# Kernel tuning notes

Measured on AMD Instinct MI355X. Metric: run time of the kernel, lower is better.

Reference implementation:

```python
import jax, jax.numpy as jnp
import numpy as np

NUM_CLASSES = 22
SKIP = 20            # skip_pixels: stride over flattened pixel index
N_STEPS = 200        # discretized steps along each voting ray
STEP = 4.0           # pixels per ray step
INLIER_T = 0.9       # inlier_threshold on direction dot-product
LABEL_T = 500.0      # label_threshold: min #pixels of a class to be valid


def _hough_forward(label_2d, vertex_pred, extents, poses, meta_data):
    B, H, W = label_2d.shape
    C = NUM_CLASSES
    HW = H * W

    # ---- strided pixel sampling (skip_pixels) ----
    idx = jnp.arange(0, HW, SKIP)                      # [P]
    P = idx.shape[0]
    ys = (idx // W).astype(jnp.float32)                # [P]
    xs = (idx % W).astype(jnp.float32)
    labels = label_2d.reshape(B, HW)[:, idx].astype(jnp.int32)   # [B,P]
    vp = vertex_pred.reshape(B, HW, C, 3)[:, idx]                # [B,P,C,3]
    # pick each pixel's predicted (dx,dy,z) for its own class label
    sel = jnp.take_along_axis(
        vp, jnp.broadcast_to(labels[:, :, None, None], (B, P, 1, 3)), axis=2
    )[:, :, 0]                                                   # [B,P,3]
    d = sel[..., :2]
    dn = d / (jnp.linalg.norm(d, axis=-1, keepdims=True) + 1e-9)  # unit dir [B,P,2]
    z = sel[..., 2]                                               # [B,P]
    fg = labels > 0                                               # foreground mask

    # ---- ray voting into per-class Hough accumulator ----
    t = (jnp.arange(N_STEPS, dtype=jnp.float32) + 1.0) * STEP     # [T]
    cx = xs[None, :, None] + dn[..., 0:1] * t[None, None, :]      # [B,P,T]
    cy = ys[None, :, None] + dn[..., 1:2] * t[None, None, :]
    cxi = jnp.round(cx).astype(jnp.int32)
    cyi = jnp.round(cy).astype(jnp.int32)
    inb = (cxi >= 0) & (cxi < W) & (cyi >= 0) & (cyi < H) & fg[..., None]
    cxi = jnp.clip(cxi, 0, W - 1)
    cyi = jnp.clip(cyi, 0, H - 1)
    bidx = jnp.arange(B, dtype=jnp.int32)[:, None, None]
    flat = ((bidx * C + labels[:, :, None]) * H + cyi) * W + cxi  # [B,P,T]
    hough = jnp.zeros((B * C * HW,), jnp.float32)
    hough = hough.at[flat.reshape(-1)].add(inb.reshape(-1).astype(jnp.float32))
    hough = hough.reshape(B, C, H, W)

    # ---- per-class peak ----
    hflat = hough.reshape(B, C, HW)
    vmax = hflat.max(-1)                               # [B,C]
    pk = jnp.argmax(hflat, axis=-1).astype(jnp.int32)  # [B,C]
    pky = (pk // W).astype(jnp.float32)
    pkx = (pk % W).astype(jnp.float32)

    # ---- validity: enough labeled pixels for the class ----
    b2 = jnp.arange(B, dtype=jnp.int32)[:, None]
    counts = jnp.zeros((B, C), jnp.float32).at[
        jnp.broadcast_to(b2, (B, HW)).reshape(-1),
        label_2d.reshape(-1).astype(jnp.int32),
    ].add(1.0)                                          # [B,C] full-res pixel counts
    cls_ids = jnp.arange(C, dtype=jnp.float32)
    valid = (counts >= LABEL_T) & (cls_ids[None, :] > 0)  # [B,C]

    # ---- inlier selection + inlier-averaged depth ----
    cx_c = jnp.take_along_axis(pkx, labels, axis=1)    # [B,P] peak of pixel's class
    cy_c = jnp.take_along_axis(pky, labels, axis=1)
    dvec = jnp.stack([cx_c - xs[None, :], cy_c - ys[None, :]], axis=-1)
    dvec = dvec / (jnp.linalg.norm(dvec, axis=-1, keepdims=True) + 1e-9)
    dot = jnp.sum(dn * dvec, axis=-1)                  # [B,P]
    inl = (fg & (dot > INLIER_T)).astype(jnp.float32)  # [B,P]
    bP = jnp.broadcast_to(b2, (B, P)).reshape(-1)
    z_sum = jnp.zeros((B, C), jnp.float32).at[bP, labels.reshape(-1)].add((z * inl).reshape(-1))
    n_inl = jnp.zeros((B, C), jnp.float32).at[bP, labels.reshape(-1)].add(inl.reshape(-1))
    depth = z_sum / jnp.maximum(n_inl, 1.0)            # [B,C]
    z_safe = jnp.where(jnp.abs(depth) > 1e-3, depth, 1.0)

    # ---- bbox from extents + intrinsics ----
    fx = meta_data[:, 0:1]                             # [B,1]
    fy = meta_data[:, 4:5]
    diam = jnp.linalg.norm(extents, axis=-1)[None, :]  # [1,C]
    half_w = 0.5 * diam * fx / z_safe
    half_h = 0.5 * diam * fy / z_safe
    vmask = valid.astype(jnp.float32)
    rois = jnp.stack([
        jnp.broadcast_to(b2.astype(jnp.float32), (B, C)),
        jnp.broadcast_to(cls_ids[None, :], (B, C)),
        pkx - half_w, pky - half_h, pkx + half_w, pky + half_h,
        vmax,
    ], axis=-1) * vmask[..., None]                     # [B,C,7]

    # ---- pose init: identity quaternion + backprojected translation ----
    Kinv = meta_data[:, 9:18].reshape(B, 3, 3)
    hom = jnp.stack([pkx, pky, jnp.ones_like(pkx)], axis=-1)      # [B,C,3]
    ray = jnp.einsum('bij,bcj->bci', Kinv, hom)
    T = depth[..., None] * ray                                    # [B,C,3]
    quat = jnp.broadcast_to(jnp.array([1.0, 0.0, 0.0, 0.0], jnp.float32), (B, C, 4))
    pose_out = jnp.concatenate([quat, T], axis=-1) * vmask[..., None]  # [B,C,7]

    return jnp.concatenate([rois, pose_out], axis=-1)  # [B,C,14]


def setup_inputs() -> dict:
    key = jax.random.key(0)
    k1, k2, k3 = jax.random.split(key, 3)
    B, H, W = 2, 480, 640
    label_2d = jax.random.randint(k1, (B, H, W), 0, NUM_CLASSES, dtype=jnp.int32)
    vertex_pred = jax.random.normal(k2, (B, H, W, 3 * NUM_CLASSES), dtype=jnp.float32)
    extents = jax.random.uniform(k3, (NUM_CLASSES, 3), minval=0.05, maxval=0.3, dtype=jnp.float32)
    poses = jnp.zeros((B, 13), jnp.float32)
    K = np.array([[1066.778, 0, 312.9869], [0, 1067.487, 241.3109], [0, 0, 1]], dtype=np.float32)
    Kinv = np.linalg.pinv(K).astype(np.float32)
    md = np.zeros((B, 48), np.float32)
    md[:, 0:9] = K.flatten()
    md[:, 9:18] = Kinv.flatten()
    meta_data = jnp.asarray(md)
    return {"label_2d": label_2d, "vertex_pred": vertex_pred, "extents": extents,
            "poses": poses, "meta_data": meta_data}


def reference(label_2d, vertex_pred, extents, poses, meta_data):
    return _hough_forward(label_2d, vertex_pred, extents, poses, meta_data)
```

## Files before the change

kernel.cpp:

```cpp
#include <hip/hip_runtime.h>
#include <math.h>

#define C_      22
#define SKIP_   20
#define NSTEP_  200
#define STEP_   4.0f
#define INL_T_  0.9f
#define LAB_T_  500
#define B_      2
#define H_      480
#define W_      640
#define HW_     (H_ * W_)
#define HWW_    (HW_ / 2)
#define P_      (HW_ / SKIP_)
#define SUB_    20
#define STEPS_PER_SUB_ (NSTEP_ / SUB_)
#define NPLANES_ (B_ * (C_ - 1))
#define CHUNKS_ 25
#define CELLS_PER_CHUNK_ (HW_ / CHUNKS_)
#define U4_PER_CHUNK_ (CELLS_PER_CHUNK_ / 8)
#define U4_PER_THREAD_ (U4_PER_CHUNK_ / 256)

#define VOTE_BLOCKS_  ((B_ * P_ * SUB_) / 256)
#define COUNT_BLOCKS_ ((B_ * HW_) / 256)

__global__ __launch_bounds__(256) void vote_count_kernel(const int* __restrict__ label,
                                                         const float* __restrict__ vp,
                                                         unsigned int* __restrict__ hough_w,
                                                         int* __restrict__ counts) {
    if (blockIdx.x < VOTE_BLOCKS_) {
        int tid = blockIdx.x * 256 + threadIdx.x;
        int pt  = tid / SUB_;
        int sub = tid - pt * SUB_;
        int b   = pt / P_;
        int pi  = pt - b * P_;
        int idx = pi * SKIP_;
        int lab = label[b * HW_ + idx];
        if (lab <= 0) return;
        float ys = (float)(idx / W_);
        float xs = (float)(idx % W_);
        const float* s = vp + ((size_t)(b * HW_ + idx) * (C_ * 3)) + lab * 3;
        float dx = s[0], dy = s[1];
        float nrm = sqrtf(__fadd_rn(__fmul_rn(dx, dx), __fmul_rn(dy, dy))) + 1e-9f;
        float dnx = dx / nrm, dny = dy / nrm;
        unsigned int* plane = hough_w + (size_t)(b * C_ + lab) * HWW_;
        int i0 = sub * STEPS_PER_SUB_;
        #pragma unroll
        for (int j = 0; j < STEPS_PER_SUB_; ++j) {
            int i = i0 + j;
            float t = (float)(i + 1) * STEP_;
            float cx = __fadd_rn(xs, __fmul_rn(dnx, t));
            float cy = __fadd_rn(ys, __fmul_rn(dny, t));
            float cxr = rintf(cx);
            float cyr = rintf(cy);
            if (cxr >= 0.0f && cxr <= (float)(W_ - 1) && cyr >= 0.0f && cyr <= (float)(H_ - 1)) {
                int cell = (int)cyr * W_ + (int)cxr;
                atomicAdd(&plane[cell >> 1], 1u << ((cell & 1) * 16));
            }
        }
    } else {
        __shared__ int h[C_];
        int cb  = blockIdx.x - VOTE_BLOCKS_;
        const int bpb = HW_ / 256;
        int b   = cb / bpb;
        int off = (cb % bpb) * 256 + threadIdx.x;
        if (threadIdx.x < C_) h[threadIdx.x] = 0;
        __syncthreads();
        int lab = label[b * HW_ + off];
        atomicAdd(&h[lab], 1);
        __syncthreads();
        if (threadIdx.x < C_) {
            int v = h[threadIdx.x];
            if (v) atomicAdd(&counts[b * C_ + threadIdx.x], v);
        }
    }
}

__global__ __launch_bounds__(256) void argmax1_kernel(const unsigned int* __restrict__ hough_w,
                                                      unsigned long long* __restrict__ key) {
    __shared__ int sv[256];
    __shared__ int si[256];
    int p     = blockIdx.x / CHUNKS_;
    int chunk = blockIdx.x % CHUNKS_;
    int b = p / (C_ - 1);
    int c = p % (C_ - 1) + 1;
    const uint4* plane4 = (const uint4*)(hough_w + (size_t)(b * C_ + c) * HWW_);
    int base4 = chunk * U4_PER_CHUNK_;
    int bv = -1;
    int bi = 0;
    #pragma unroll
    for (int j = 0; j < U4_PER_THREAD_; ++j) {
        int f4 = base4 + j * 256 + threadIdx.x;
        uint4 w = plane4[f4];
        int i0 = f4 * 8;
        int v;
        v = (int)(w.x & 0xFFFFu); if (v > bv) { bv = v; bi = i0;     }
        v = (int)(w.x >> 16);     if (v > bv) { bv = v; bi = i0 + 1; }
        v = (int)(w.y & 0xFFFFu); if (v > bv) { bv = v; bi = i0 + 2; }
        v = (int)(w.y >> 16);     if (v > bv) { bv = v; bi = i0 + 3; }
        v = (int)(w.z & 0xFFFFu); if (v > bv) { bv = v; bi = i0 + 4; }
        v = (int)(w.z >> 16);     if (v > bv) { bv = v; bi = i0 + 5; }
        v = (int)(w.w & 0xFFFFu); if (v > bv) { bv = v; bi = i0 + 6; }
        v = (int)(w.w >> 16);     if (v > bv) { bv = v; bi = i0 + 7; }
    }
    sv[threadIdx.x] = bv; si[threadIdx.x] = bi;
    __syncthreads();
    for (int s = 128; s > 0; s >>= 1) {
        if (threadIdx.x < s) {
            int ov = sv[threadIdx.x + s], oi = si[threadIdx.x + s];
            if (ov > sv[threadIdx.x] || (ov == sv[threadIdx.x] && oi < si[threadIdx.x])) {
                sv[threadIdx.x] = ov; si[threadIdx.x] = oi;
            }
        }
        __syncthreads();
    }
    if (threadIdx.x == 0) {
        unsigned long long k = ((unsigned long long)(unsigned int)sv[0] << 32)
                             | (unsigned long long)(0xFFFFFFFFu - (unsigned int)si[0]);
        atomicMax(&key[b * C_ + c], k);
    }
}

__global__ __launch_bounds__(256) void inlier_kernel(const int* __restrict__ label,
                                                     const float* __restrict__ vp,
                                                     const unsigned long long* __restrict__ key,
                                                     float* __restrict__ z_sum,
                                                     float* __restrict__ n_inl) {
    __shared__ float zs[C_];
    __shared__ float ns[C_];
    const int bpb = P_ / 256;
    int b  = blockIdx.x / bpb;
    int pi = (blockIdx.x % bpb) * 256 + threadIdx.x;
    if (threadIdx.x < C_) { zs[threadIdx.x] = 0.0f; ns[threadIdx.x] = 0.0f; }
    __syncthreads();
    int idx = pi * SKIP_;
    int lab = label[b * HW_ + idx];
    if (lab > 0) {
        float ys = (float)(idx / W_);
        float xs = (float)(idx % W_);
        const float* s = vp + ((size_t)(b * HW_ + idx) * (C_ * 3)) + lab * 3;
        float dx = s[0], dy = s[1], z = s[2];
        float nrm = sqrtf(__fadd_rn(__fmul_rn(dx, dx), __fmul_rn(dy, dy))) + 1e-9f;
        float dnx = dx / nrm, dny = dy / nrm;
        unsigned long long k = key[b * C_ + lab];
        int pkv = (int)(0xFFFFFFFFu - (unsigned int)(k & 0xFFFFFFFFull));
        float pkx = (float)(pkv % W_), pky = (float)(pkv / W_);
        float dvx = __fsub_rn(pkx, xs), dvy = __fsub_rn(pky, ys);
        float nrm2 = sqrtf(__fadd_rn(__fmul_rn(dvx, dvx), __fmul_rn(dvy, dvy))) + 1e-9f;
        dvx /= nrm2; dvy /= nrm2;
        float dot = __fadd_rn(__fmul_rn(dnx, dvx), __fmul_rn(dny, dvy));
        if (dot > INL_T_) {
            atomicAdd(&zs[lab], z);
            atomicAdd(&ns[lab], 1.0f);
        }
    }
    __syncthreads();
    if (threadIdx.x < C_) {
        if (ns[threadIdx.x] != 0.0f) {
            atomicAdd(&z_sum[b * C_ + threadIdx.x], zs[threadIdx.x]);
            atomicAdd(&n_inl[b * C_ + threadIdx.x], ns[threadIdx.x]);
        }
    }
}

__global__ __launch_bounds__(64) void finalize_kernel(const int* __restrict__ counts,
                                                      const unsigned long long* __restrict__ key,
                                                      const float* __restrict__ z_sum,
                                                      const float* __restrict__ n_inl,
                                                      const float* __restrict__ extents,
                                                      const float* __restrict__ meta,
                                                      float* __restrict__ out) {
    int t = threadIdx.x;
    if (t >= B_ * C_) return;
    int b = t / C_, c = t % C_;
    float* o = out + t * 14;
    bool valid = (counts[t] >= LAB_T_) && (c > 0);
    if (!valid) {
        #pragma unroll
        for (int k = 0; k < 14; ++k) o[k] = 0.0f;
        return;
    }
    float depth = z_sum[t] / fmaxf(n_inl[t], 1.0f);
    float z_safe = (fabsf(depth) > 0.001f) ? depth : 1.0f;
    float fx = meta[b * 48 + 0];
    float fy = meta[b * 48 + 4];
    const float* e = extents + c * 3;
    float diam = sqrtf(e[0]*e[0] + e[1]*e[1] + e[2]*e[2]);
    unsigned long long k = key[t];
    float vmax = (float)(unsigned int)(k >> 32);
    int pkv = (int)(0xFFFFFFFFu - (unsigned int)(k & 0xFFFFFFFFull));
    float pkx = (float)(pkv % W_), pky = (float)(pkv / W_);
    float half_w = ((0.5f * diam) * fx) / z_safe;
    float half_h = ((0.5f * diam) * fy) / z_safe;
    o[0] = (float)b;
    o[1] = (float)c;
    o[2] = pkx - half_w;
    o[3] = pky - half_h;
    o[4] = pkx + half_w;
    o[5] = pky + half_h;
    o[6] = vmax;
    const float* Ki = meta + b * 48 + 9;
    float rx = Ki[0]*pkx + Ki[1]*pky + Ki[2];
    float ry = Ki[3]*pkx + Ki[4]*pky + Ki[5];
    float rz = Ki[6]*pkx + Ki[7]*pky + Ki[8];
    o[7]  = 1.0f;
    o[8]  = 0.0f;
    o[9]  = 0.0f;
    o[10] = 0.0f;
    o[11] = depth * rx;
    o[12] = depth * ry;
    o[13] = depth * rz;
}

extern "C" void kernel_launch(void* const* d_in, const int* in_sizes, int n_in,
                              void* d_out, int out_size, void* d_ws, size_t ws_size,
                              hipStream_t stream) {
    const int*   label   = (const int*)d_in[0];
    const float* vp      = (const float*)d_in[1];
    const float* extents = (const float*)d_in[2];
    const float* meta    = (const float*)d_in[4];
    float* out = (float*)d_out;

    char* ws = (char*)d_ws;
    unsigned int* hough_w = (unsigned int*)ws;
    size_t off = (size_t)B_ * C_ * HWW_ * sizeof(unsigned int);
    unsigned long long* key = (unsigned long long*)(ws + off); off += B_ * C_ * sizeof(unsigned long long);
    int*   counts = (int*)(ws + off);   off += B_ * C_ * sizeof(int);
    float* z_sum  = (float*)(ws + off); off += B_ * C_ * sizeof(float);
    float* n_inl  = (float*)(ws + off); off += B_ * C_ * sizeof(float);
    size_t zero_bytes = off;

    hipMemsetAsync(d_ws, 0, zero_bytes, stream);

    vote_count_kernel<<<VOTE_BLOCKS_ + COUNT_BLOCKS_, 256, 0, stream>>>(label, vp, hough_w, counts);
    argmax1_kernel<<<NPLANES_ * CHUNKS_, 256, 0, stream>>>(hough_w, key);
    inlier_kernel<<<(B_ * P_) / 256, 256, 0, stream>>>(label, vp, key, z_sum, n_inl);
    finalize_kernel<<<1, 64, 0, stream>>>(counts, key, z_sum, n_inl, extents, meta, out);
}
```

Baseline: 309.6 us.

## Bin ray segments per tile and rasterize votes in shared memory

Replaces the global per-class Hough accumulator with a two-pass scheme. The first pass walks each ray and appends each run of consecutive steps that stays inside one 64x64 tile to a per-(plane, tile) list. The second pass rebuilds each tile's votes with LDS atomics and finds the argmax there. This removes the large global accumulator memset and the scattered global atomics. The cost is a list-building pass, and per-tile lists capped at 1024 runs that would silently drop votes if a tile overflows.

```diff
diff --git a/kernel.cpp b/kernel.cpp
--- a/kernel.cpp
+++ b/kernel.cpp
@@ -11,56 +11,80 @@
 #define H_      480
 #define W_      640
 #define HW_     (H_ * W_)
-#define HWW_    (HW_ / 2)
 #define P_      (HW_ / SKIP_)
-#define SUB_    20
-#define STEPS_PER_SUB_ (NSTEP_ / SUB_)
-#define NPLANES_ (B_ * (C_ - 1))
-#define CHUNKS_ 25
-#define CELLS_PER_CHUNK_ (HW_ / CHUNKS_)
-#define U4_PER_CHUNK_ (CELLS_PER_CHUNK_ / 8)
-#define U4_PER_THREAD_ (U4_PER_CHUNK_ / 256)
-
-#define VOTE_BLOCKS_  ((B_ * P_ * SUB_) / 256)
+
+#define TS_       64
+#define TILES_X_  (W_ / TS_)
+#define TILES_Y_  (H_ / TS_)
+#define NTILES_Y_ 8
+#define NTILES_   (TILES_X_ * NTILES_Y_)
+#define NPLANES_  (B_ * (C_ - 1))
+#define NPT_      (NPLANES_ * NTILES_)
+#define CAP_      1024
+
+#define SUB_A_    4
+#define SEG_LEN_  (NSTEP_ / SUB_A_)
+#define PA_BLOCKS_    ((B_ * P_ * SUB_A_) / 256)
 #define COUNT_BLOCKS_ ((B_ * HW_) / 256)
 
-__global__ __launch_bounds__(256) void vote_count_kernel(const int* __restrict__ label,
-                                                         const float* __restrict__ vp,
-                                                         unsigned int* __restrict__ hough_w,
-                                                         int* __restrict__ counts) {
-    if (blockIdx.x < VOTE_BLOCKS_) {
+__device__ __forceinline__ void emit_run(unsigned int* cnt, uint4* lists, int pt,
+                                         int xi, int yi, int i0, int i1,
+                                         float dnx, float dny) {
+    unsigned slot = atomicAdd(&cnt[pt], 1u);
+    if (slot < CAP_) {
+        uint4 r;
+        r.x = (unsigned)xi | ((unsigned)yi << 16);
+        r.y = (unsigned)i0 | ((unsigned)i1 << 8);
+        r.z = __float_as_uint(dnx);
+        r.w = __float_as_uint(dny);
+        lists[(size_t)pt * CAP_ + slot] = r;
+    }
+}
+
+__global__ __launch_bounds__(256) void binray_count_kernel(const int* __restrict__ label,
+                                                           const float* __restrict__ vp,
+                                                           unsigned int* __restrict__ cnt,
+                                                           uint4* __restrict__ lists,
+                                                           int* __restrict__ counts) {
+    if (blockIdx.x < PA_BLOCKS_) {
         int tid = blockIdx.x * 256 + threadIdx.x;
-        int pt  = tid / SUB_;
-        int sub = tid - pt * SUB_;
+        int pt  = tid >> 2;
+        int sub = tid & 3;
         int b   = pt / P_;
         int pi  = pt - b * P_;
         int idx = pi * SKIP_;
         int lab = label[b * HW_ + idx];
         if (lab <= 0) return;
-        float ys = (float)(idx / W_);
-        float xs = (float)(idx % W_);
+        int xi = idx % W_, yi = idx / W_;
+        float xs = (float)xi, ys = (float)yi;
         const float* s = vp + ((size_t)(b * HW_ + idx) * (C_ * 3)) + lab * 3;
         float dx = s[0], dy = s[1];
         float nrm = sqrtf(__fadd_rn(__fmul_rn(dx, dx), __fmul_rn(dy, dy))) + 1e-9f;
         float dnx = dx / nrm, dny = dy / nrm;
-        unsigned int* plane = hough_w + (size_t)(b * C_ + lab) * HWW_;
-        int i0 = sub * STEPS_PER_SUB_;
-        #pragma unroll
-        for (int j = 0; j < STEPS_PER_SUB_; ++j) {
-            int i = i0 + j;
+        int base = (b * (C_ - 1) + (lab - 1)) * NTILES_;
+        int curTile = -1, runStart = 0;
+        int iBeg = sub * SEG_LEN_, iEnd = iBeg + SEG_LEN_;
+        for (int i = iBeg; i < iEnd; ++i) {
             float t = (float)(i + 1) * STEP_;
             float cx = __fadd_rn(xs, __fmul_rn(dnx, t));
             float cy = __fadd_rn(ys, __fmul_rn(dny, t));
             float cxr = rintf(cx);
             float cyr = rintf(cy);
-            if (cxr >= 0.0f && cxr <= (float)(W_ - 1) && cyr >= 0.0f && cyr <= (float)(H_ - 1)) {
-                int cell = (int)cyr * W_ + (int)cxr;
-                atomicAdd(&plane[cell >> 1], 1u << ((cell & 1) * 16));
+            int tile = -1;
+            if (cxr >= 0.0f && cxr <= (float)(W_ - 1) && cyr >= 0.0f && cyr <= (float)(H_ - 1))
+                tile = (((int)cyr) >> 6) * TILES_X_ + (((int)cxr) >> 6);
+            if (tile != curTile) {
+                if (curTile >= 0)
+                    emit_run(cnt, lists, base + curTile, xi, yi, runStart, i - 1, dnx, dny);
+                curTile = tile;
+                runStart = i;
             }
         }
+        if (curTile >= 0)
+            emit_run(cnt, lists, base + curTile, xi, yi, runStart, iEnd - 1, dnx, dny);
     } else {
         __shared__ int h[C_];
-        int cb  = blockIdx.x - VOTE_BLOCKS_;
+        int cb  = blockIdx.x - PA_BLOCKS_;
         const int bpb = HW_ / 256;
         int b   = cb / bpb;
         int off = (cb % bpb) * 256 + threadIdx.x;
@@ -76,38 +100,56 @@
     }
 }
 
-__global__ __launch_bounds__(256) void argmax1_kernel(const unsigned int* __restrict__ hough_w,
-                                                      unsigned long long* __restrict__ key) {
-    __shared__ int sv[256];
-    __shared__ int si[256];
-    int p     = blockIdx.x / CHUNKS_;
-    int chunk = blockIdx.x % CHUNKS_;
+__global__ __launch_bounds__(256) void raster_argmax_kernel(const unsigned int* __restrict__ cnt,
+                                                            const uint4* __restrict__ lists,
+                                                            unsigned long long* __restrict__ key) {
+    __shared__ unsigned int tile[TS_ * TS_];
+    __shared__ unsigned int sv[256];
+    __shared__ int          si[256];
+    int ptile = blockIdx.x;
+    int p  = ptile / NTILES_;
+    int tl = ptile % NTILES_;
     int b = p / (C_ - 1);
     int c = p % (C_ - 1) + 1;
-    const uint4* plane4 = (const uint4*)(hough_w + (size_t)(b * C_ + c) * HWW_);
-    int base4 = chunk * U4_PER_CHUNK_;
-    int bv = -1;
-    int bi = 0;
+    int x0 = (tl % TILES_X_) * TS_;
+    int y0 = (tl / TILES_X_) * TS_;
+    for (int j = threadIdx.x; j < TS_ * TS_; j += 256) tile[j] = 0u;
+    __syncthreads();
+    int n = (int)cnt[ptile];
+    if (n > CAP_) n = CAP_;
+    const uint4* lst = lists + (size_t)ptile * CAP_;
+    int wave = threadIdx.x >> 6, lane = threadIdx.x & 63;
+    for (int r = wave; r < n; r += 4) {
+        uint4 rec = lst[r];
+        int i0 = (int)(rec.y & 0xFFu), i1 = (int)((rec.y >> 8) & 0xFFu);
+        int i = i0 + lane;
+        if (i <= i1) {
+            float xs = (float)(rec.x & 0xFFFFu);
+            float ys = (float)(rec.x >> 16);
+            float dnx = __uint_as_float(rec.z);
+            float dny = __uint_as_float(rec.w);
+            float t = (float)(i + 1) * STEP_;
+            float cx = __fadd_rn(xs, __fmul_rn(dnx, t));
+            float cy = __fadd_rn(ys, __fmul_rn(dny, t));
+            int lx = (int)rintf(cx) - x0;
+            int ly = (int)rintf(cy) - y0;
+            atomicAdd(&tile[ly * TS_ + lx], 1u);
+        }
+    }
+    __syncthreads();
+    int start = threadIdx.x * 16;
+    unsigned bv = tile[start];
+    int bloc = start;
     #pragma unroll
-    for (int j = 0; j < U4_PER_THREAD_; ++j) {
-        int f4 = base4 + j * 256 + threadIdx.x;
-        uint4 w = plane4[f4];
-        int i0 = f4 * 8;
-        int v;
-        v = (int)(w.x & 0xFFFFu); if (v > bv) { bv = v; bi = i0;     }
-        v = (int)(w.x >> 16);     if (v > bv) { bv = v; bi = i0 + 1; }
-        v = (int)(w.y & 0xFFFFu); if (v > bv) { bv = v; bi = i0 + 2; }
-        v = (int)(w.y >> 16);     if (v > bv) { bv = v; bi = i0 + 3; }
-        v = (int)(w.z & 0xFFFFu); if (v > bv) { bv = v; bi = i0 + 4; }
-        v = (int)(w.z >> 16);     if (v > bv) { bv = v; bi = i0 + 5; }
-        v = (int)(w.w & 0xFFFFu); if (v > bv) { bv = v; bi = i0 + 6; }
-        v = (int)(w.w >> 16);     if (v > bv) { bv = v; bi = i0 + 7; }
-    }
-    sv[threadIdx.x] = bv; si[threadIdx.x] = bi;
+    for (int j = 1; j < 16; ++j) {
+        unsigned v = tile[start + j];
+        if (v > bv) { bv = v; bloc = start + j; }
+    }
+    sv[threadIdx.x] = bv; si[threadIdx.x] = bloc;
     __syncthreads();
     for (int s = 128; s > 0; s >>= 1) {
         if (threadIdx.x < s) {
-            int ov = sv[threadIdx.x + s], oi = si[threadIdx.x + s];
+            unsigned ov = sv[threadIdx.x + s]; int oi = si[threadIdx.x + s];
             if (ov > sv[threadIdx.x] || (ov == sv[threadIdx.x] && oi < si[threadIdx.x])) {
                 sv[threadIdx.x] = ov; si[threadIdx.x] = oi;
             }
@@ -115,8 +157,10 @@
         __syncthreads();
     }
     if (threadIdx.x == 0) {
-        unsigned long long k = ((unsigned long long)(unsigned int)sv[0] << 32)
-                             | (unsigned long long)(0xFFFFFFFFu - (unsigned int)si[0]);
+        int ly = si[0] >> 6, lx = si[0] & 63;
+        unsigned gidx = (unsigned)((y0 + ly) * W_ + (x0 + lx));
+        unsigned long long k = ((unsigned long long)sv[0] << 32)
+                             | (unsigned long long)(0xFFFFFFFFu - gidx);
         atomicMax(&key[b * C_ + c], k);
     }
 }
@@ -222,18 +266,19 @@
     float* out = (float*)d_out;
 
     char* ws = (char*)d_ws;
-    unsigned int* hough_w = (unsigned int*)ws;
-    size_t off = (size_t)B_ * C_ * HWW_ * sizeof(unsigned int);
+    size_t off = 0;
+    unsigned int* cnt = (unsigned int*)(ws + off);          off += NPT_ * sizeof(unsigned int);
     unsigned long long* key = (unsigned long long*)(ws + off); off += B_ * C_ * sizeof(unsigned long long);
     int*   counts = (int*)(ws + off);   off += B_ * C_ * sizeof(int);
     float* z_sum  = (float*)(ws + off); off += B_ * C_ * sizeof(float);
     float* n_inl  = (float*)(ws + off); off += B_ * C_ * sizeof(float);
     size_t zero_bytes = off;
+    uint4* lists = (uint4*)(ws + off);
 
     hipMemsetAsync(d_ws, 0, zero_bytes, stream);
 
-    vote_count_kernel<<<VOTE_BLOCKS_ + COUNT_BLOCKS_, 256, 0, stream>>>(label, vp, hough_w, counts);
-    argmax1_kernel<<<NPLANES_ * CHUNKS_, 256, 0, stream>>>(hough_w, key);
+    binray_count_kernel<<<PA_BLOCKS_ + COUNT_BLOCKS_, 256, 0, stream>>>(label, vp, cnt, lists, counts);
+    raster_argmax_kernel<<<NPT_, 256, 0, stream>>>(cnt, lists, key);
     inlier_kernel<<<(B_ * P_) / 256, 256, 0, stream>>>(label, vp, key, z_sum, n_inl);
     finalize_kernel<<<1, 64, 0, stream>>>(counts, key, z_sum, n_inl, extents, meta, out);
 }
```

Result: faster. 288.1 us (-6.9%).
